# Optimization experiments

Measured on AMD Instinct MI355X. Metric: run time of the kernel, lower is better.

The kernel has to match this reference:

```python
import jax, jax.numpy as jnp
import numpy as np

N_ATOMS = 20000
N_CG = 1000
N_EDGES = 200000
FEAT = 128
N_RBF = 20
N_CONV = 3
CUTOFF = 5.0
EPS = 1e-15


def swish(x):
    return x * jax.nn.sigmoid(x)


def preprocess_r(r):
    # r: (n, 3) -> dist (n,), unit (n, 3)
    d = jnp.sqrt((r * r + EPS).sum(-1))
    return d, r / d[:, None]


def dist_embed(d, W, b):
    # PainnRadialBasis (learnable_k=False) + Dense + cosine envelope
    k = jnp.arange(1, N_RBF + 1, dtype=d.dtype)
    rbf = jnp.sin(k[None, :] * jnp.pi * d[:, None] / CUTOFF) / d[:, None]
    env = 0.5 * (jnp.cos(jnp.pi * d / CUTOFF) + 1.0) * (d < CUTOFF).astype(d.dtype)
    return (rbf @ W + b) * env[:, None]


def scatter_mean(x, idx, n):
    s = jax.ops.segment_sum(x, idx, num_segments=n)
    cnt = jax.ops.segment_sum(jnp.ones(idx.shape[0], x.dtype), idx, num_segments=n)
    cnt = jnp.maximum(cnt, 1.0)
    return s / cnt.reshape((n,) + (1,) * (x.ndim - 1))


def cg_encoder(z, xyz, cg_xyz, mapping, nbr_list, embed,
               msg_W1, msg_b1, msg_W2, msg_b2, msg_distW, msg_distb,
               upd_U, upd_V, upd_W1, upd_b1, upd_W2, upd_b2,
               cg_W1, cg_b1, cg_W2, cg_b2, cg_distW, cg_distb):
    s = embed[z]                                     # (N, F)
    v = jnp.zeros((s.shape[0], FEAT, 3), s.dtype)    # (N, F, 3)
    src, dst = nbr_list[:, 0], nbr_list[:, 1]
    r_ij = xyz[dst] - xyz[src]
    r_iI = xyz - cg_xyz[mapping]
    d_ij, u_ij = preprocess_r(r_ij)
    d_iI, u_iI = preprocess_r(r_iI)

    S_I = None
    V_I = None
    for i in range(N_CONV):
        # ---- MessageBlock ----
        phi = swish(s @ msg_W1[i] + msg_b1[i]) @ msg_W2[i] + msg_b2[i]          # (N, 3F)
        w_s = dist_embed(d_ij, msg_distW[i], msg_distb[i])                      # (E, 3F)
        inv = (phi[dst] * w_s).reshape(-1, 3, FEAT)                             # (E, 3, F)
        dv_ij = inv[:, 2, :, None] * u_ij[:, None, :] + inv[:, 0, :, None] * v[dst]
        s = s + jax.ops.segment_sum(inv[:, 1, :], src, num_segments=N_ATOMS)
        v = v + jax.ops.segment_sum(dv_ij, src, num_segments=N_ATOMS)
        # ---- UpdateBlock ----
        u_v = jnp.einsum('nfd,fg->ngd', v, upd_U[i])
        v_v = jnp.einsum('nfd,fg->ngd', v, upd_V[i])
        v_v_norm = jnp.sqrt((v_v * v_v + EPS).sum(-1))                          # (N, F)
        stack = swish(jnp.concatenate([s, v_v_norm], -1) @ upd_W1[i] + upd_b1[i]) @ upd_W2[i] + upd_b2[i]
        a_vv = stack[:, :FEAT, None]
        a_sv = stack[:, FEAT:2 * FEAT]
        a_ss = stack[:, 2 * FEAT:]
        v = v + u_v * a_vv
        s = s + (u_v * v_v).sum(-1) * a_sv + a_ss
        # ---- init CG features after first conv ----
        if i == 0:
            S_I = scatter_mean(s, mapping, N_CG)
            V_I = jnp.zeros((N_CG, FEAT, 3), s.dtype)
        # ---- ContractiveMessageBlock ----
        phi_cg = swish(s @ cg_W1[i] + cg_b1[i]) @ cg_W2[i] + cg_b2[i]           # (N, 3F)
        w_cg = dist_embed(d_iI, cg_distW[i], cg_distb[i])
        inv_cg = (phi_cg * w_cg).reshape(-1, 3, FEAT)
        dv_iI = inv_cg[:, 2, :, None] * u_iI[:, None, :] + inv_cg[:, 0, :, None] * v
        S_I = S_I + scatter_mean(inv_cg[:, 1, :], mapping, N_CG)
        V_I = V_I + scatter_mean(dv_iI, mapping, N_CG)
    return S_I


def setup_inputs() -> dict:
    key = jax.random.key(0)
    ks = jax.random.split(key, 20)
    p = lambda i, shape: jax.random.normal(ks[i], shape, jnp.float32) * 0.05
    return {
        'z': jax.random.randint(ks[0], (N_ATOMS,), 1, 100),
        'xyz': jax.random.normal(ks[1], (N_ATOMS, 3), jnp.float32),
        'cg_xyz': jax.random.normal(ks[2], (N_CG, 3), jnp.float32),
        'mapping': jax.random.randint(ks[3], (N_ATOMS,), 0, N_CG),
        'nbr_list': jax.random.randint(ks[4], (N_EDGES, 2), 0, N_ATOMS),
        'embed': p(5, (100, FEAT)).at[0].set(0.0),  # padding_idx=0
        'msg_W1': p(6, (N_CONV, FEAT, FEAT)), 'msg_b1': jnp.zeros((N_CONV, FEAT)),
        'msg_W2': p(7, (N_CONV, FEAT, 3 * FEAT)), 'msg_b2': jnp.zeros((N_CONV, 3 * FEAT)),
        'msg_distW': p(8, (N_CONV, N_RBF, 3 * FEAT)), 'msg_distb': jnp.zeros((N_CONV, 3 * FEAT)),
        'upd_U': p(9, (N_CONV, FEAT, FEAT)), 'upd_V': p(10, (N_CONV, FEAT, FEAT)),
        'upd_W1': p(11, (N_CONV, 2 * FEAT, FEAT)), 'upd_b1': jnp.zeros((N_CONV, FEAT)),
        'upd_W2': p(12, (N_CONV, FEAT, 3 * FEAT)), 'upd_b2': jnp.zeros((N_CONV, 3 * FEAT)),
        'cg_W1': p(13, (N_CONV, FEAT, FEAT)), 'cg_b1': jnp.zeros((N_CONV, FEAT)),
        'cg_W2': p(14, (N_CONV, FEAT, 3 * FEAT)), 'cg_b2': jnp.zeros((N_CONV, 3 * FEAT)),
        'cg_distW': p(15, (N_CONV, N_RBF, 3 * FEAT)), 'cg_distb': jnp.zeros((N_CONV, 3 * FEAT)),
    }


def reference(z, xyz, cg_xyz, mapping, nbr_list, embed,
              msg_W1, msg_b1, msg_W2, msg_b2, msg_distW, msg_distb,
              upd_U, upd_V, upd_W1, upd_b1, upd_W2, upd_b2,
              cg_W1, cg_b1, cg_W2, cg_b2, cg_distW, cg_distb):
    return cg_encoder(z, xyz, cg_xyz, mapping, nbr_list, embed,
                      msg_W1, msg_b1, msg_W2, msg_b2, msg_distW, msg_distb,
                      upd_U, upd_V, upd_W1, upd_b1, upd_W2, upd_b2,
                      cg_W1, cg_b1, cg_W2, cg_b2, cg_distW, cg_distb)
```

## Files before the change

kernel.cpp:

```cpp
#include <hip/hip_runtime.h>
#include <math.h>

#define N_ATOMS 20000
#define N_CG    1000
#define N_EDGES 200000
#define FEAT    128
#define NRBF    20
#define NCONV   3
#define CUTOFF  5.0f
#define PLANE   (N_ATOMS * FEAT)
#define PI_F    3.14159265358979323846f
#define LDH     130

#define PACK_PER_CONV 212992

typedef __attribute__((ext_vector_type(8))) short bf16x8;
typedef __attribute__((ext_vector_type(4))) float f32x4;

__device__ __forceinline__ void split2(float x, ushort& h, ushort& l)
{
    unsigned u  = __float_as_uint(x);
    unsigned hb = (u + 0x7FFFu + ((u >> 16) & 1u)) & 0xFFFF0000u;
    float    hf = __uint_as_float(hb);
    float    lf = x - hf;
    unsigned ul = __float_as_uint(lf);
    h = (ushort)(hb >> 16);
    l = (ushort)((ul + 0x7FFFu + ((ul >> 16) & 1u)) >> 16);
}

__device__ __forceinline__ void splitv8(const float* hv, bf16x8& ah, bf16x8& al)
{
#pragma unroll
    for (int j = 0; j < 8; ++j) {
        ushort h, l;
        split2(hv[j], h, l);
        ah[j] = (short)h; al[j] = (short)l;
    }
}

#define MFMA3(ACC, AH_, AL_, BH_, BL_)                                              \
    ACC = __builtin_amdgcn_mfma_f32_16x16x32_bf16(AH_, BH_, ACC, 0, 0, 0);          \
    ACC = __builtin_amdgcn_mfma_f32_16x16x32_bf16(AH_, BL_, ACC, 0, 0, 0);          \
    ACC = __builtin_amdgcn_mfma_f32_16x16x32_bf16(AL_, BH_, ACC, 0, 0, 0);

template<int K1, int N2>
__global__ __launch_bounds__(256)
void mlp_fused(const ushort* __restrict__ AH, const ushort* __restrict__ AL,
               const ushort* __restrict__ B1h, const ushort* __restrict__ B1l,
               const float* __restrict__ b1,
               const ushort* __restrict__ B2h, const ushort* __restrict__ B2l,
               const float* __restrict__ b2, int bcol0,
               float* __restrict__ C)
{
    __shared__ float Hs[32 * LDH];
    const int tid  = threadIdx.x;
    const int lane = tid & 63;
    const int w    = tid >> 6;
    const int wm   = w & 1, wn = w >> 1;
    const int m0   = blockIdx.x * 32;
    const int l15  = lane & 15;
    const int koff = (lane >> 4) * 8;
    const int rowb = wm * 16;
    const int q4   = (lane >> 4) * 4;

    f32x4 acc1[4];
#pragma unroll
    for (int j = 0; j < 4; ++j) acc1[j] = (f32x4){0.f, 0.f, 0.f, 0.f};
    for (int k0 = 0; k0 < K1; k0 += 32) {
        size_t aa = (size_t)(m0 + rowb + l15) * K1 + k0 + koff;
        bf16x8 ah = *reinterpret_cast<const bf16x8*>(AH + aa);
        bf16x8 al = *reinterpret_cast<const bf16x8*>(AL + aa);
#pragma unroll
        for (int nf = 0; nf < 4; ++nf) {
            size_t ba = (size_t)(wn * 64 + nf * 16 + l15) * K1 + k0 + koff;
            bf16x8 bh = *reinterpret_cast<const bf16x8*>(B1h + ba);
            bf16x8 bl = *reinterpret_cast<const bf16x8*>(B1l + ba);
            MFMA3(acc1[nf], ah, al, bh, bl);
        }
    }
#pragma unroll
    for (int nf = 0; nf < 4; ++nf) {
        int col = wn * 64 + nf * 16 + l15;
        float bv = b1[col];
#pragma unroll
        for (int r = 0; r < 4; ++r) {
            float x = acc1[nf][r] + bv;
            x = x / (1.f + __expf(-x));
            Hs[(rowb + q4 + r) * LDH + col] = x;
        }
    }
    __syncthreads();

    constexpr int NF2  = N2 / 32;
    constexpr int WCOL = N2 / 2;
    f32x4 acc2[NF2];
#pragma unroll
    for (int j = 0; j < NF2; ++j) acc2[j] = (f32x4){0.f, 0.f, 0.f, 0.f};
    for (int k0 = 0; k0 < 128; k0 += 32) {
        const float* hp = &Hs[(rowb + l15) * LDH + k0 + koff];
        float hv[8];
#pragma unroll
        for (int j = 0; j < 4; ++j) hv[j] = hp[j];
#pragma unroll
        for (int j = 0; j < 4; ++j) hv[4 + j] = hp[4 + j];
        bf16x8 ah, al;
        splitv8(hv, ah, al);
#pragma unroll
        for (int nf = 0; nf < NF2; ++nf) {
            size_t ba = (size_t)(wn * WCOL + nf * 16 + l15) * 128 + k0 + koff;
            bf16x8 bh = *reinterpret_cast<const bf16x8*>(B2h + ba);
            bf16x8 bl = *reinterpret_cast<const bf16x8*>(B2l + ba);
            MFMA3(acc2[nf], ah, al, bh, bl);
        }
    }
#pragma unroll
    for (int nf = 0; nf < NF2; ++nf) {
        int col = wn * WCOL + nf * 16 + l15;
        float bv = b2 ? b2[bcol0 + col] : 0.f;
#pragma unroll
        for (int r = 0; r < 4; ++r) {
            int row = m0 + rowb + q4 + r;
            C[(size_t)row * N2 + col] = acc2[nf][r] + bv;
        }
    }
}

__global__ __launch_bounds__(256)
void gemm_vnorm(const ushort* __restrict__ vHp, const ushort* __restrict__ vLp,
                const ushort* __restrict__ Bh, const ushort* __restrict__ Bl,
                float* __restrict__ vv,
                ushort* __restrict__ CcatH, ushort* __restrict__ CcatL)
{
    const int tid  = threadIdx.x;
    const int lane = tid & 63;
    const int w    = tid >> 6;
    const int wm   = w & 1, wn = w >> 1;
    const int m0   = blockIdx.x * 32;
    const int l15  = lane & 15;
    const int koff = (lane >> 4) * 8;
    const int rowb = wm * 16;
    const int q4   = (lane >> 4) * 4;

    f32x4 acc[3][4];
#pragma unroll
    for (int d = 0; d < 3; ++d)
#pragma unroll
        for (int j = 0; j < 4; ++j) acc[d][j] = (f32x4){0.f, 0.f, 0.f, 0.f};

    for (int k0 = 0; k0 < 128; k0 += 32) {
        bf16x8 ah[3], al[3];
#pragma unroll
        for (int d = 0; d < 3; ++d) {
            size_t aa = (size_t)d * PLANE + (size_t)(m0 + rowb + l15) * 128 + k0 + koff;
            ah[d] = *reinterpret_cast<const bf16x8*>(vHp + aa);
            al[d] = *reinterpret_cast<const bf16x8*>(vLp + aa);
        }
#pragma unroll
        for (int nf = 0; nf < 4; ++nf) {
            size_t ba = (size_t)(wn * 64 + nf * 16 + l15) * 128 + k0 + koff;
            bf16x8 bh = *reinterpret_cast<const bf16x8*>(Bh + ba);
            bf16x8 bl = *reinterpret_cast<const bf16x8*>(Bl + ba);
#pragma unroll
            for (int d = 0; d < 3; ++d) {
                MFMA3(acc[d][nf], ah[d], al[d], bh, bl);
            }
        }
    }
#pragma unroll
    for (int nf = 0; nf < 4; ++nf) {
        int col = wn * 64 + nf * 16 + l15;
#pragma unroll
        for (int r = 0; r < 4; ++r) {
            int row = m0 + rowb + q4 + r;
            int idx = row * FEAT + col;
            float x = acc[0][nf][r], y = acc[1][nf][r], z = acc[2][nf][r];
            vv[idx] = x; vv[PLANE + idx] = y; vv[2 * PLANE + idx] = z;
            float nrm = sqrtf(x * x + y * y + z * z + 3e-15f);
            ushort h, l;
            split2(nrm, h, l);
            CcatH[(size_t)row * 256 + 128 + col] = h;
            CcatL[(size_t)row * 256 + 128 + col] = l;
        }
    }
}

__global__ __launch_bounds__(256)
void gemm_u_update(const ushort* __restrict__ vHp, const ushort* __restrict__ vLp,
                   const ushort* __restrict__ Bh, const ushort* __restrict__ Bl,
                   const float* __restrict__ vv, const float* __restrict__ stack,
                   float* __restrict__ s, float* __restrict__ v,
                   ushort* __restrict__ sH, ushort* __restrict__ sL)
{
    const int tid  = threadIdx.x;
    const int lane = tid & 63;
    const int w    = tid >> 6;
    const int wm   = w & 1, wn = w >> 1;
    const int m0   = blockIdx.x * 32;
    const int l15  = lane & 15;
    const int koff = (lane >> 4) * 8;
    const int rowb = wm * 16;
    const int q4   = (lane >> 4) * 4;

    f32x4 acc[3][4];
#pragma unroll
    for (int d = 0; d < 3; ++d)
#pragma unroll
        for (int j = 0; j < 4; ++j) acc[d][j] = (f32x4){0.f, 0.f, 0.f, 0.f};

    for (int k0 = 0; k0 < 128; k0 += 32) {
        bf16x8 ah[3], al[3];
#pragma unroll
        for (int d = 0; d < 3; ++d) {
            size_t aa = (size_t)d * PLANE + (size_t)(m0 + rowb + l15) * 128 + k0 + koff;
            ah[d] = *reinterpret_cast<const bf16x8*>(vHp + aa);
            al[d] = *reinterpret_cast<const bf16x8*>(vLp + aa);
        }
#pragma unroll
        for (int nf = 0; nf < 4; ++nf) {
            size_t ba = (size_t)(wn * 64 + nf * 16 + l15) * 128 + k0 + koff;
            bf16x8 bh = *reinterpret_cast<const bf16x8*>(Bh + ba);
            bf16x8 bl = *reinterpret_cast<const bf16x8*>(Bl + ba);
#pragma unroll
            for (int d = 0; d < 3; ++d) {
                MFMA3(acc[d][nf], ah[d], al[d], bh, bl);
            }
        }
    }
    ushort* vHo = const_cast<ushort*>(vHp);
    ushort* vLo = const_cast<ushort*>(vLp);
#pragma unroll
    for (int nf = 0; nf < 4; ++nf) {
        int col = wn * 64 + nf * 16 + l15;
#pragma unroll
        for (int r = 0; r < 4; ++r) {
            int row = m0 + rowb + q4 + r;
            int idx = row * FEAT + col;
            const float* st = stack + (size_t)row * 384 + col;
            float avv = st[0], asv = st[128], ass = st[256];
            float u0 = acc[0][nf][r], u1 = acc[1][nf][r], u2 = acc[2][nf][r];
            float w0 = vv[idx], w1 = vv[PLANE + idx], w2 = vv[2 * PLANE + idx];
            float dot = u0 * w0 + u1 * w1 + u2 * w2;
            float n0 = v[idx]             + u0 * avv;
            float n1 = v[PLANE + idx]     + u1 * avv;
            float n2 = v[2 * PLANE + idx] + u2 * avv;
            v[idx] = n0; v[PLANE + idx] = n1; v[2 * PLANE + idx] = n2;
            ushort h, l;
            split2(n0, h, l); vHo[idx] = h;             vLo[idx] = l;
            split2(n1, h, l); vHo[PLANE + idx] = h;     vLo[PLANE + idx] = l;
            split2(n2, h, l); vHo[2 * PLANE + idx] = h; vLo[2 * PLANE + idx] = l;
            float ns = s[idx] + dot * asv + ass;
            s[idx] = ns;
            split2(ns, h, l); sH[idx] = h; sL[idx] = l;
        }
    }
}

__global__ void k_pack_all(const float* __restrict__ msg_W1, const float* __restrict__ msg_W2,
                           const float* __restrict__ upd_V,  const float* __restrict__ upd_W1,
                           const float* __restrict__ upd_W2, const float* __restrict__ upd_U,
                           const float* __restrict__ cg_W1,  const float* __restrict__ cg_W2,
                           ushort* __restrict__ Bh, ushort* __restrict__ Bl)
{
    const int wid = blockIdx.y, conv = blockIdx.z;
    const float* W; int K, N, ldw, col0; size_t off;
    switch (wid) {
        case 0: W = msg_W1 + (size_t)conv * 16384; K = 128; N = 128; ldw = 128; col0 = 0;   off = 0;      break;
        case 1: W = msg_W2 + (size_t)conv * 49152; K = 128; N = 384; ldw = 384; col0 = 0;   off = 16384;  break;
        case 2: W = upd_V  + (size_t)conv * 16384; K = 128; N = 128; ldw = 128; col0 = 0;   off = 65536;  break;
        case 3: W = upd_W1 + (size_t)conv * 32768; K = 256; N = 128; ldw = 128; col0 = 0;   off = 81920;  break;
        case 4: W = upd_W2 + (size_t)conv * 49152; K = 128; N = 384; ldw = 384; col0 = 0;   off = 114688; break;
        case 5: W = upd_U  + (size_t)conv * 16384; K = 128; N = 128; ldw = 128; col0 = 0;   off = 163840; break;
        case 6: W = cg_W1  + (size_t)conv * 16384; K = 128; N = 128; ldw = 128; col0 = 0;   off = 180224; break;
        default:W = cg_W2  + (size_t)conv * 49152; K = 128; N = 128; ldw = 384; col0 = 128; off = 196608; break;
    }
    off += (size_t)conv * PACK_PER_CONV;
    int idx = blockIdx.x * 256 + threadIdx.x;
    if (idx >= K * N) return;
    int k = idx & (K - 1);
    int n = idx >> ((K == 256) ? 8 : 7);
    ushort h, l;
    split2(W[(size_t)k * ldw + col0 + n], h, l);
    Bh[off + (size_t)n * K + k] = h;
    Bl[off + (size_t)n * K + k] = l;
}

__global__ void k_s_init(const int* __restrict__ z, const float* __restrict__ embed,
                         float* __restrict__ s, ushort* __restrict__ sH, ushort* __restrict__ sL)
{
    int idx = blockIdx.x * blockDim.x + threadIdx.x;
    if (idx >= PLANE) return;
    int n = idx >> 7, g = idx & 127;
    float e = embed[z[n] * FEAT + g];
    s[idx] = e;
    ushort h, l;
    split2(e, h, l);
    sH[idx] = h; sL[idx] = l;
}

__global__ void k_atom_geo(const int* __restrict__ mapping,
                           const float* __restrict__ xyz, const float* __restrict__ cg_xyz,
                           float* __restrict__ rbf_a, float* __restrict__ env_a,
                           float* __restrict__ cnt)
{
    int n = blockIdx.x * blockDim.x + threadIdx.x;
    if (n >= N_ATOMS) return;
    int m = mapping[n];
    float dx = xyz[n * 3 + 0] - cg_xyz[m * 3 + 0];
    float dy = xyz[n * 3 + 1] - cg_xyz[m * 3 + 1];
    float dz = xyz[n * 3 + 2] - cg_xyz[m * 3 + 2];
    float d = sqrtf(dx * dx + dy * dy + dz * dz + 3e-15f);
    float env = (d < CUTOFF) ? 0.5f * (cosf(PI_F * d / CUTOFF) + 1.f) : 0.f;
    env_a[n] = env;
    float s = env / d;
#pragma unroll
    for (int k = 0; k < NRBF; ++k)
        rbf_a[n * NRBF + k] = sinf((k + 1) * PI_F * d / CUTOFF) * s;
    atomicAdd(&cnt[m], 1.f);
}

__global__ void k_deg(const int* __restrict__ nbr, int* __restrict__ deg)
{
    int e = blockIdx.x * blockDim.x + threadIdx.x;
    if (e < N_EDGES) atomicAdd(&deg[nbr[2 * e]], 1);
}

__global__ __launch_bounds__(1024)
void k_scan(const int* __restrict__ deg, int* __restrict__ rowptr)
{
    __shared__ int sh[1024];
    const int chunk = (N_ATOMS + 1023) / 1024;
    int t = threadIdx.x;
    int base = t * chunk;
    int sum = 0;
    for (int i = 0; i < chunk; ++i) {
        int idx = base + i;
        if (idx < N_ATOMS) sum += deg[idx];
    }
    sh[t] = sum;
    __syncthreads();
    for (int off = 1; off < 1024; off <<= 1) {
        int val = (t >= off) ? sh[t - off] : 0;
        __syncthreads();
        sh[t] += val;
        __syncthreads();
    }
    int run = (t == 0) ? 0 : sh[t - 1];
    for (int i = 0; i < chunk; ++i) {
        int idx = base + i;
        if (idx < N_ATOMS) { rowptr[idx] = run; run += deg[idx]; }
    }
}

__global__ void k_fill(const int* __restrict__ nbr, const float* __restrict__ xyz,
                       const int* __restrict__ rowptr, int* __restrict__ cursor,
                       int* __restrict__ rec_dst, float4* __restrict__ rec_u4,
                       float* __restrict__ rec_rbf)
{
    int e = blockIdx.x * blockDim.x + threadIdx.x;
    if (e >= N_EDGES) return;
    int src = nbr[2 * e], dst = nbr[2 * e + 1];
    int pos = atomicAdd(&cursor[src], 1);
    int q = rowptr[src] + pos;
    float dx = xyz[dst * 3 + 0] - xyz[src * 3 + 0];
    float dy = xyz[dst * 3 + 1] - xyz[src * 3 + 1];
    float dz = xyz[dst * 3 + 2] - xyz[src * 3 + 2];
    float d = sqrtf(dx * dx + dy * dy + dz * dz + 3e-15f);
    float env = (d < CUTOFF) ? 0.5f * (cosf(PI_F * d / CUTOFF) + 1.f) : 0.f;
    rec_dst[q] = dst;
    rec_u4[q] = make_float4(dx / d, dy / d, dz / d, env);
    float sc = env / d;
#pragma unroll
    for (int k = 0; k < NRBF; ++k)
        rec_rbf[(size_t)q * NRBF + k] = sinf((k + 1) * PI_F * d / CUTOFF) * sc;
}

#define EDGE_BLOCKS 2500
__global__ __launch_bounds__(512, 2)
void k_edge_seg(const int* __restrict__ rowptr, const int* __restrict__ deg,
                const int* __restrict__ rec_dst, const float4* __restrict__ rec_u4,
                const float* __restrict__ rec_rbf,
                const float* __restrict__ phi,
                const float* __restrict__ v_in, float* __restrict__ v_out,
                float* __restrict__ s,
                ushort* __restrict__ vH, ushort* __restrict__ vL,
                ushort* __restrict__ CcatH, ushort* __restrict__ CcatL,
                const float* __restrict__ distW, const float* __restrict__ distb)
{
    const int tid    = threadIdx.x;
    const int slot   = tid >> 7;
    const int f      = tid & 127;
    const int slot_g = blockIdx.x * 4 + slot;
    const int nslots = EDGE_BLOCKS * 4;

    float wx[21], wy[21], wz[21];
#pragma unroll
    for (int k = 0; k < NRBF; ++k) {
        wx[k] = distW[k * 384 + f];
        wy[k] = distW[k * 384 + 128 + f];
        wz[k] = distW[k * 384 + 256 + f];
    }
    wx[20] = distb[f];
    wy[20] = distb[128 + f];
    wz[20] = distb[256 + f];
#pragma unroll
    for (int k = 0; k < 21; ++k) {
        asm volatile("" : "+v"(wx[k]), "+v"(wy[k]), "+v"(wz[k]));
    }

    for (int a = slot_g; a < N_ATOMS; a += nslots) {
        const int beg = rowptr[a];
        const int end = beg + deg[a];
        float s_acc = 0.f, vx = 0.f, vy = 0.f, vz = 0.f;

        for (int p = beg; p < end; p += 2) {
            const int  has2 = (p + 1 < end);
            const int  p1   = has2 ? p + 1 : p;
            const float m1  = has2 ? 1.f : 0.f;

            float4 u40 = rec_u4[p];
            float4 u41 = rec_u4[p1];
            int dst0 = rec_dst[p];
            int dst1 = rec_dst[p1];

            const float* ph0 = phi + (size_t)dst0 * 384 + f;
            const float* ph1 = phi + (size_t)dst1 * 384 + f;
            float p00 = ph0[0], p01 = ph0[128], p02 = ph0[256];
            float p10 = ph1[0], p11 = ph1[128], p12 = ph1[256];
            int di0 = dst0 * FEAT + f;
            int di1 = dst1 * FEAT + f;
            float v0x = v_in[di0], v0y = v_in[PLANE + di0], v0z = v_in[2 * PLANE + di0];
            float v1x = v_in[di1], v1y = v_in[PLANE + di1], v1z = v_in[2 * PLANE + di1];
            const float4* rb0 = reinterpret_cast<const float4*>(rec_rbf + (size_t)p  * NRBF);
            const float4* rb1 = reinterpret_cast<const float4*>(rec_rbf + (size_t)p1 * NRBF);
            float4 a0 = rb0[0], a1 = rb0[1], a2 = rb0[2], a3 = rb0[3], a4 = rb0[4];
            float4 b0 = rb1[0], b1 = rb1[1], b2 = rb1[2], b3 = rb1[3], b4 = rb1[4];

            const float rr0[21] = {a0.x, a0.y, a0.z, a0.w, a1.x, a1.y, a1.z, a1.w,
                                   a2.x, a2.y, a2.z, a2.w, a3.x, a3.y, a3.z, a3.w,
                                   a4.x, a4.y, a4.z, a4.w, u40.w};
            const float rr1[21] = {b0.x, b0.y, b0.z, b0.w, b1.x, b1.y, b1.z, b1.w,
                                   b2.x, b2.y, b2.z, b2.w, b3.x, b3.y, b3.z, b3.w,
                                   b4.x, b4.y, b4.z, b4.w, u41.w};
            float w00 = 0.f, w01 = 0.f, w02 = 0.f;
            float w10 = 0.f, w11 = 0.f, w12 = 0.f;
#pragma unroll
            for (int k = 0; k < 21; ++k) {
                w00 += rr0[k] * wx[k];
                w01 += rr0[k] * wy[k];
                w02 += rr0[k] * wz[k];
                w10 += rr1[k] * wx[k];
                w11 += rr1[k] * wy[k];
                w12 += rr1[k] * wz[k];
            }
            float i00 = p00 * w00, i01 = p01 * w01, i02 = p02 * w02;
            float i10 = (p10 * w10) * m1, i11 = (p11 * w11) * m1, i12 = (p12 * w12) * m1;
            vx += i02 * u40.x + i00 * v0x;
            vy += i02 * u40.y + i00 * v0y;
            vz += i02 * u40.z + i00 * v0z;
            s_acc += i01;
            vx += i12 * u41.x + i10 * v1x;
            vy += i12 * u41.y + i10 * v1y;
            vz += i12 * u41.z + i10 * v1z;
            s_acc += i11;
        }

        int si = a * FEAT + f;
        float ns = s[si] + s_acc;
        s[si] = ns;
        float nx = v_in[si]             + vx;
        float ny = v_in[PLANE + si]     + vy;
        float nz = v_in[2 * PLANE + si] + vz;
        v_out[si] = nx; v_out[PLANE + si] = ny; v_out[2 * PLANE + si] = nz;
        ushort h, l;
        split2(nx, h, l); vH[si] = h;             vL[si] = l;
        split2(ny, h, l); vH[PLANE + si] = h;     vL[PLANE + si] = l;
        split2(nz, h, l); vH[2 * PLANE + si] = h; vL[2 * PLANE + si] = l;
        split2(ns, h, l);
        CcatH[(size_t)a * 256 + f] = h;
        CcatL[(size_t)a * 256 + f] = l;
    }
}

__global__ __launch_bounds__(128)
void k_cg_msg(const int* __restrict__ mapping, const float* __restrict__ phi_mid,
              const float* __restrict__ rbf_a, const float* __restrict__ env_a,
              const float* __restrict__ distW, const float* __restrict__ distb,
              const float* __restrict__ s_add, float* __restrict__ S_acc)
{
    int n = blockIdx.x;
    float env = env_a[n];
    int f = threadIdx.x;
    if (env == 0.f && s_add == nullptr) return;
    float val = s_add ? s_add[n * FEAT + f] : 0.f;
    if (env != 0.f) {
        __shared__ float sh_rbf[NRBF];
        if (f < NRBF) sh_rbf[f] = rbf_a[n * NRBF + f];
        __syncthreads();
        float w1 = 0.f;
#pragma unroll
        for (int k = 0; k < NRBF; ++k)
            w1 += sh_rbf[k] * distW[k * 384 + 128 + f];
        w1 += distb[128 + f] * env;
        val += phi_mid[n * FEAT + f] * w1;
    }
    atomicAdd(&S_acc[mapping[n] * FEAT + f], val);
}

__global__ void k_finalize(const float* __restrict__ S_acc, const float* __restrict__ cnt,
                           float* __restrict__ out, int add)
{
    int idx = blockIdx.x * blockDim.x + threadIdx.x;
    if (idx >= N_CG * FEAT) return;
    float val = S_acc[idx] / fmaxf(cnt[idx >> 7], 1.f);
    if (add) out[idx] += val;
    else     out[idx] = val;
}

extern "C" void kernel_launch(void* const* d_in, const int* in_sizes, int n_in,
                              void* d_out, int out_size, void* d_ws, size_t ws_size,
                              hipStream_t stream)
{
    const int*   z        = (const int*)d_in[0];
    const float* xyz      = (const float*)d_in[1];
    const float* cg_xyz   = (const float*)d_in[2];
    const int*   mapping  = (const int*)d_in[3];
    const int*   nbr      = (const int*)d_in[4];
    const float* embed    = (const float*)d_in[5];
    const float* msg_W1   = (const float*)d_in[6];
    const float* msg_b1   = (const float*)d_in[7];
    const float* msg_W2   = (const float*)d_in[8];
    const float* msg_b2   = (const float*)d_in[9];
    const float* msg_dW   = (const float*)d_in[10];
    const float* msg_db   = (const float*)d_in[11];
    const float* upd_U    = (const float*)d_in[12];
    const float* upd_V    = (const float*)d_in[13];
    const float* upd_W1   = (const float*)d_in[14];
    const float* upd_b1   = (const float*)d_in[15];
    const float* upd_W2   = (const float*)d_in[16];
    const float* upd_b2   = (const float*)d_in[17];
    const float* cg_W1    = (const float*)d_in[18];
    const float* cg_b1    = (const float*)d_in[19];
    const float* cg_W2    = (const float*)d_in[20];
    const float* cg_b2    = (const float*)d_in[21];
    const float* cg_dW    = (const float*)d_in[22];
    const float* cg_db    = (const float*)d_in[23];
    float* out = (float*)d_out;

    float* ws = (float*)d_ws;
    size_t o = 0;
    float* s      = ws + o; o += PLANE;
    float* vA     = ws + o; o += 3 * PLANE;
    float* vB     = ws + o; o += 3 * PLANE;
    float* uv     = ws + o; o += PLANE;
    float* phi    = ws + o; o += (size_t)N_ATOMS * 384;
    float* Cpk    = ws + o; o += (size_t)N_ATOMS * 256;
    float* spk    = ws + o; o += PLANE;
    float* vpk    = ws + o; o += 3 * PLANE;
    float4* rec_u4 = (float4*)(ws + o); o += (size_t)N_EDGES * 4;
    float* rec_rbf = ws + o; o += (size_t)N_EDGES * NRBF;
    int*   rec_dst = (int*)(ws + o); o += N_EDGES;
    float* rbf_a  = ws + o; o += (size_t)N_ATOMS * NRBF;
    float* env_a  = ws + o; o += N_ATOMS;
    float* cnt    = ws + o; o += N_CG;
    float* S_acc  = ws + o; o += N_CG * FEAT;
    int*   deg    = (int*)(ws + o); o += N_ATOMS;
    int*   rowptr = (int*)(ws + o); o += N_ATOMS;
    int*   cursor = (int*)(ws + o); o += N_ATOMS;
    ushort* packH = (ushort*)(ws + o); o += (size_t)NCONV * PACK_PER_CONV / 2;
    ushort* packL = (ushort*)(ws + o); o += (size_t)NCONV * PACK_PER_CONV / 2;

    ushort* CcatH = (ushort*)Cpk; ushort* CcatL = CcatH + (size_t)N_ATOMS * 256;
    ushort* sH = (ushort*)spk;  ushort* sL = sH + PLANE;
    ushort* vH = (ushort*)vpk;  ushort* vL = vH + 3 * PLANE;

    hipMemsetAsync(vA, 0, sizeof(float) * 3 * PLANE, stream);
    hipMemsetAsync(cnt, 0, sizeof(float) * N_CG, stream);
    hipMemsetAsync(deg, 0, sizeof(int) * N_ATOMS, stream);
    hipMemsetAsync(cursor, 0, sizeof(int) * N_ATOMS, stream);
    k_pack_all<<<dim3(192, 8, 3), 256, 0, stream>>>(msg_W1, msg_W2, upd_V, upd_W1,
                                                    upd_W2, upd_U, cg_W1, cg_W2,
                                                    packH, packL);
    k_s_init<<<(PLANE + 255) / 256, 256, 0, stream>>>(z, embed, s, sH, sL);
    k_atom_geo<<<(N_ATOMS + 255) / 256, 256, 0, stream>>>(mapping, xyz, cg_xyz,
                                                          rbf_a, env_a, cnt);
    k_deg<<<(N_EDGES + 255) / 256, 256, 0, stream>>>(nbr, deg);
    k_scan<<<1, 1024, 0, stream>>>(deg, rowptr);
    k_fill<<<(N_EDGES + 255) / 256, 256, 0, stream>>>(nbr, xyz, rowptr, cursor,
                                                      rec_dst, rec_u4, rec_rbf);

    float* v_cur = vA;
    float* v_nxt = vB;

    for (int i = 0; i < NCONV; ++i) {
        const float* mb1 = msg_b1 + (size_t)i * FEAT;
        const float* mb2 = msg_b2 + (size_t)i * 384;
        const float* mdW = msg_dW + (size_t)i * NRBF * 384;
        const float* mdb = msg_db + (size_t)i * 384;
        const float* ub1 = upd_b1 + (size_t)i * FEAT;
        const float* ub2 = upd_b2 + (size_t)i * 384;
        const float* cb1 = cg_b1  + (size_t)i * FEAT;
        const float* cb2 = cg_b2  + (size_t)i * 384;
        const float* cdW = cg_dW  + (size_t)i * NRBF * 384;
        const float* cdb = cg_db  + (size_t)i * 384;
        const size_t pb  = (size_t)i * PACK_PER_CONV;

        mlp_fused<128, 384><<<625, 256, 0, stream>>>(
            sH, sL, packH + pb + 0, packL + pb + 0, mb1,
            packH + pb + 16384, packL + pb + 16384, mb2, 0, phi);
        k_edge_seg<<<EDGE_BLOCKS, 512, 0, stream>>>(rowptr, deg, rec_dst, rec_u4,
                                                    rec_rbf, phi, v_cur, v_nxt, s,
                                                    vH, vL, CcatH, CcatL, mdW, mdb);
        float* vv = v_cur;

        gemm_vnorm<<<625, 256, 0, stream>>>(vH, vL, packH + pb + 65536,
                                            packL + pb + 65536, vv, CcatH, CcatL);
        mlp_fused<256, 384><<<625, 256, 0, stream>>>(
            CcatH, CcatL, packH + pb + 81920, packL + pb + 81920, ub1,
            packH + pb + 114688, packL + pb + 114688, ub2, 0, phi);
        gemm_u_update<<<625, 256, 0, stream>>>(vH, vL, packH + pb + 163840,
                                               packL + pb + 163840, vv, phi,
                                               s, v_nxt, sH, sL);

        mlp_fused<128, 128><<<625, 256, 0, stream>>>(
            sH, sL, packH + pb + 180224, packL + pb + 180224, cb1,
            packH + pb + 196608, packL + pb + 196608, cb2, 128, uv);
        hipMemsetAsync(S_acc, 0, sizeof(float) * N_CG * FEAT, stream);
        k_cg_msg<<<N_ATOMS, 128, 0, stream>>>(mapping, uv, rbf_a, env_a, cdW, cdb,
                                              (i == 0) ? s : nullptr, S_acc);
        k_finalize<<<(N_CG * FEAT + 255) / 256, 256, 0, stream>>>(S_acc, cnt, out,
                                                                  i == 0 ? 0 : 1);

        float* tmp = v_nxt;
        v_nxt = v_cur;
        v_cur = tmp;
    }
}
```

Measured before the change: 1.363 ms.

## Fuse update block into one kernel and drop fp32 v buffers for bf16 split pairs

```diff
diff --git a/kernel.cpp b/kernel.cpp
--- a/kernel.cpp
+++ b/kernel.cpp
@@ -28,6 +28,12 @@
     l = (ushort)((ul + 0x7FFFu + ((ul >> 16) & 1u)) >> 16);
 }
 
+__device__ __forceinline__ float recon(const ushort* __restrict__ H,
+                                       const ushort* __restrict__ L, size_t i)
+{
+    return __uint_as_float((unsigned)H[i] << 16) + __uint_as_float((unsigned)L[i] << 16);
+}
+
 __device__ __forceinline__ void splitv8(const float* hv, bf16x8& ah, bf16x8& al)
 {
 #pragma unroll
@@ -126,11 +132,23 @@
 }
 
 __global__ __launch_bounds__(256)
-void gemm_vnorm(const ushort* __restrict__ vHp, const ushort* __restrict__ vLp,
-                const ushort* __restrict__ Bh, const ushort* __restrict__ Bl,
-                float* __restrict__ vv,
-                ushort* __restrict__ CcatH, ushort* __restrict__ CcatL)
-{
+void k_update_mega(const ushort* __restrict__ vHp, const ushort* __restrict__ vLp,
+                   const ushort* __restrict__ catH, const ushort* __restrict__ catL,
+                   const ushort* __restrict__ BVh, const ushort* __restrict__ BVl,
+                   const ushort* __restrict__ W1h, const ushort* __restrict__ W1l,
+                   const float*  __restrict__ b1,
+                   const ushort* __restrict__ W2h, const ushort* __restrict__ W2l,
+                   const float*  __restrict__ b2,
+                   const ushort* __restrict__ BUh, const ushort* __restrict__ BUl,
+                   float* __restrict__ s,
+                   ushort* __restrict__ sH, ushort* __restrict__ sL)
+{
+    __shared__ __align__(16) char smem[16640 + 49152];
+    float*  Hs  = (float*)smem;
+    float*  stk = (float*)(smem + 16640);
+    ushort* nH  = (ushort*)(smem + 16640);
+    ushort* nL  = (ushort*)(smem + 16640 + 8192);
+
     const int tid  = threadIdx.x;
     const int lane = tid & 63;
     const int w    = tid >> 6;
@@ -141,12 +159,14 @@
     const int rowb = wm * 16;
     const int q4   = (lane >> 4) * 4;
 
-    f32x4 acc[3][4];
+    f32x4 accV[3][4], accU[3][4];
 #pragma unroll
     for (int d = 0; d < 3; ++d)
 #pragma unroll
-        for (int j = 0; j < 4; ++j) acc[d][j] = (f32x4){0.f, 0.f, 0.f, 0.f};
-
+        for (int j = 0; j < 4; ++j) {
+            accV[d][j] = (f32x4){0.f, 0.f, 0.f, 0.f};
+            accU[d][j] = (f32x4){0.f, 0.f, 0.f, 0.f};
+        }
     for (int k0 = 0; k0 < 128; k0 += 32) {
         bf16x8 ah[3], al[3];
 #pragma unroll
@@ -158,11 +178,17 @@
 #pragma unroll
         for (int nf = 0; nf < 4; ++nf) {
             size_t ba = (size_t)(wn * 64 + nf * 16 + l15) * 128 + k0 + koff;
-            bf16x8 bh = *reinterpret_cast<const bf16x8*>(Bh + ba);
-            bf16x8 bl = *reinterpret_cast<const bf16x8*>(Bl + ba);
+            bf16x8 bvh = *reinterpret_cast<const bf16x8*>(BVh + ba);
+            bf16x8 bvl = *reinterpret_cast<const bf16x8*>(BVl + ba);
+            bf16x8 buh = *reinterpret_cast<const bf16x8*>(BUh + ba);
+            bf16x8 bul = *reinterpret_cast<const bf16x8*>(BUl + ba);
 #pragma unroll
             for (int d = 0; d < 3; ++d) {
-                MFMA3(acc[d][nf], ah[d], al[d], bh, bl);
+                MFMA3(accV[d][nf], ah[d], al[d], bvh, bvl);
+            }
+#pragma unroll
+            for (int d = 0; d < 3; ++d) {
+                MFMA3(accU[d][nf], ah[d], al[d], buh, bul);
             }
         }
     }
@@ -171,61 +197,81 @@
         int col = wn * 64 + nf * 16 + l15;
 #pragma unroll
         for (int r = 0; r < 4; ++r) {
-            int row = m0 + rowb + q4 + r;
-            int idx = row * FEAT + col;
-            float x = acc[0][nf][r], y = acc[1][nf][r], z = acc[2][nf][r];
-            vv[idx] = x; vv[PLANE + idx] = y; vv[2 * PLANE + idx] = z;
+            int lrow = rowb + q4 + r;
+            float x = accV[0][nf][r], y = accV[1][nf][r], z = accV[2][nf][r];
             float nrm = sqrtf(x * x + y * y + z * z + 3e-15f);
             ushort h, l;
             split2(nrm, h, l);
-            CcatH[(size_t)row * 256 + 128 + col] = h;
-            CcatL[(size_t)row * 256 + 128 + col] = l;
-        }
-    }
-}
-
-__global__ __launch_bounds__(256)
-void gemm_u_update(const ushort* __restrict__ vHp, const ushort* __restrict__ vLp,
-                   const ushort* __restrict__ Bh, const ushort* __restrict__ Bl,
-                   const float* __restrict__ vv, const float* __restrict__ stack,
-                   float* __restrict__ s, float* __restrict__ v,
-                   ushort* __restrict__ sH, ushort* __restrict__ sL)
-{
-    const int tid  = threadIdx.x;
-    const int lane = tid & 63;
-    const int w    = tid >> 6;
-    const int wm   = w & 1, wn = w >> 1;
-    const int m0   = blockIdx.x * 32;
-    const int l15  = lane & 15;
-    const int koff = (lane >> 4) * 8;
-    const int rowb = wm * 16;
-    const int q4   = (lane >> 4) * 4;
-
-    f32x4 acc[3][4];
-#pragma unroll
-    for (int d = 0; d < 3; ++d)
-#pragma unroll
-        for (int j = 0; j < 4; ++j) acc[d][j] = (f32x4){0.f, 0.f, 0.f, 0.f};
-
+            nH[lrow * 128 + col] = h;
+            nL[lrow * 128 + col] = l;
+        }
+    }
+    __syncthreads();
+
+    f32x4 acc1[4];
+#pragma unroll
+    for (int j = 0; j < 4; ++j) acc1[j] = (f32x4){0.f, 0.f, 0.f, 0.f};
+    for (int k0 = 0; k0 < 256; k0 += 32) {
+        bf16x8 ah, al;
+        if (k0 < 128) {
+            size_t aa = (size_t)(m0 + rowb + l15) * 128 + k0 + koff;
+            ah = *reinterpret_cast<const bf16x8*>(catH + aa);
+            al = *reinterpret_cast<const bf16x8*>(catL + aa);
+        } else {
+            int la = (rowb + l15) * 128 + (k0 - 128) + koff;
+            ah = *reinterpret_cast<const bf16x8*>(nH + la);
+            al = *reinterpret_cast<const bf16x8*>(nL + la);
+        }
+#pragma unroll
+        for (int nf = 0; nf < 4; ++nf) {
+            size_t ba = (size_t)(wn * 64 + nf * 16 + l15) * 256 + k0 + koff;
+            bf16x8 bh = *reinterpret_cast<const bf16x8*>(W1h + ba);
+            bf16x8 bl = *reinterpret_cast<const bf16x8*>(W1l + ba);
+            MFMA3(acc1[nf], ah, al, bh, bl);
+        }
+    }
+#pragma unroll
+    for (int nf = 0; nf < 4; ++nf) {
+        int col = wn * 64 + nf * 16 + l15;
+        float bv = b1[col];
+#pragma unroll
+        for (int r = 0; r < 4; ++r) {
+            float x = acc1[nf][r] + bv;
+            x = x / (1.f + __expf(-x));
+            Hs[(rowb + q4 + r) * LDH + col] = x;
+        }
+    }
+    __syncthreads();
+
+    f32x4 acc2[12];
+#pragma unroll
+    for (int j = 0; j < 12; ++j) acc2[j] = (f32x4){0.f, 0.f, 0.f, 0.f};
     for (int k0 = 0; k0 < 128; k0 += 32) {
-        bf16x8 ah[3], al[3];
-#pragma unroll
-        for (int d = 0; d < 3; ++d) {
-            size_t aa = (size_t)d * PLANE + (size_t)(m0 + rowb + l15) * 128 + k0 + koff;
-            ah[d] = *reinterpret_cast<const bf16x8*>(vHp + aa);
-            al[d] = *reinterpret_cast<const bf16x8*>(vLp + aa);
-        }
-#pragma unroll
-        for (int nf = 0; nf < 4; ++nf) {
-            size_t ba = (size_t)(wn * 64 + nf * 16 + l15) * 128 + k0 + koff;
-            bf16x8 bh = *reinterpret_cast<const bf16x8*>(Bh + ba);
-            bf16x8 bl = *reinterpret_cast<const bf16x8*>(Bl + ba);
-#pragma unroll
-            for (int d = 0; d < 3; ++d) {
-                MFMA3(acc[d][nf], ah[d], al[d], bh, bl);
-            }
-        }
-    }
+        const float* hp = &Hs[(rowb + l15) * LDH + k0 + koff];
+        float hv[8];
+#pragma unroll
+        for (int j = 0; j < 8; ++j) hv[j] = hp[j];
+        bf16x8 ah, al;
+        splitv8(hv, ah, al);
+#pragma unroll
+        for (int nf = 0; nf < 12; ++nf) {
+            size_t ba = (size_t)(wn * 192 + nf * 16 + l15) * 128 + k0 + koff;
+            bf16x8 bh = *reinterpret_cast<const bf16x8*>(W2h + ba);
+            bf16x8 bl = *reinterpret_cast<const bf16x8*>(W2l + ba);
+            MFMA3(acc2[nf], ah, al, bh, bl);
+        }
+    }
+#pragma unroll
+    for (int nf = 0; nf < 12; ++nf) {
+        int col = wn * 192 + nf * 16 + l15;
+        float bv = b2[col];
+#pragma unroll
+        for (int r = 0; r < 4; ++r) {
+            stk[(rowb + q4 + r) * 384 + col] = acc2[nf][r] + bv;
+        }
+    }
+    __syncthreads();
+
     ushort* vHo = const_cast<ushort*>(vHp);
     ushort* vLo = const_cast<ushort*>(vLp);
 #pragma unroll
@@ -233,17 +279,18 @@
         int col = wn * 64 + nf * 16 + l15;
 #pragma unroll
         for (int r = 0; r < 4; ++r) {
-            int row = m0 + rowb + q4 + r;
-            int idx = row * FEAT + col;
-            const float* st = stack + (size_t)row * 384 + col;
-            float avv = st[0], asv = st[128], ass = st[256];
-            float u0 = acc[0][nf][r], u1 = acc[1][nf][r], u2 = acc[2][nf][r];
-            float w0 = vv[idx], w1 = vv[PLANE + idx], w2 = vv[2 * PLANE + idx];
+            int lrow = rowb + q4 + r;
+            int row  = m0 + lrow;
+            int idx  = row * FEAT + col;
+            float avv = stk[lrow * 384 + col];
+            float asv = stk[lrow * 384 + 128 + col];
+            float ass = stk[lrow * 384 + 256 + col];
+            float u0 = accU[0][nf][r], u1 = accU[1][nf][r], u2 = accU[2][nf][r];
+            float w0 = accV[0][nf][r], w1 = accV[1][nf][r], w2 = accV[2][nf][r];
             float dot = u0 * w0 + u1 * w1 + u2 * w2;
-            float n0 = v[idx]             + u0 * avv;
-            float n1 = v[PLANE + idx]     + u1 * avv;
-            float n2 = v[2 * PLANE + idx] + u2 * avv;
-            v[idx] = n0; v[PLANE + idx] = n1; v[2 * PLANE + idx] = n2;
+            float n0 = recon(vHp, vLp, idx)                    + u0 * avv;
+            float n1 = recon(vHp, vLp, (size_t)PLANE + idx)    + u1 * avv;
+            float n2 = recon(vHp, vLp, (size_t)2 * PLANE + idx)+ u2 * avv;
             ushort h, l;
             split2(n0, h, l); vHo[idx] = h;             vLo[idx] = l;
             split2(n1, h, l); vHo[PLANE + idx] = h;     vLo[PLANE + idx] = l;
@@ -380,10 +427,10 @@
                 const int* __restrict__ rec_dst, const float4* __restrict__ rec_u4,
                 const float* __restrict__ rec_rbf,
                 const float* __restrict__ phi,
-                const float* __restrict__ v_in, float* __restrict__ v_out,
+                const ushort* __restrict__ vHi, const ushort* __restrict__ vLi,
+                ushort* __restrict__ vHo, ushort* __restrict__ vLo,
                 float* __restrict__ s,
-                ushort* __restrict__ vH, ushort* __restrict__ vL,
-                ushort* __restrict__ CcatH, ushort* __restrict__ CcatL,
+                ushort* __restrict__ catH, ushort* __restrict__ catL,
                 const float* __restrict__ distW, const float* __restrict__ distb)
 {
     const int tid    = threadIdx.x;
@@ -426,10 +473,14 @@
             const float* ph1 = phi + (size_t)dst1 * 384 + f;
             float p00 = ph0[0], p01 = ph0[128], p02 = ph0[256];
             float p10 = ph1[0], p11 = ph1[128], p12 = ph1[256];
-            int di0 = dst0 * FEAT + f;
-            int di1 = dst1 * FEAT + f;
-            float v0x = v_in[di0], v0y = v_in[PLANE + di0], v0z = v_in[2 * PLANE + di0];
-            float v1x = v_in[di1], v1y = v_in[PLANE + di1], v1z = v_in[2 * PLANE + di1];
+            size_t di0 = (size_t)dst0 * FEAT + f;
+            size_t di1 = (size_t)dst1 * FEAT + f;
+            float v0x = recon(vHi, vLi, di0);
+            float v0y = recon(vHi, vLi, PLANE + di0);
+            float v0z = recon(vHi, vLi, 2 * (size_t)PLANE + di0);
+            float v1x = recon(vHi, vLi, di1);
+            float v1y = recon(vHi, vLi, PLANE + di1);
+            float v1z = recon(vHi, vLi, 2 * (size_t)PLANE + di1);
             const float4* rb0 = reinterpret_cast<const float4*>(rec_rbf + (size_t)p  * NRBF);
             const float4* rb1 = reinterpret_cast<const float4*>(rec_rbf + (size_t)p1 * NRBF);
             float4 a0 = rb0[0], a1 = rb0[1], a2 = rb0[2], a3 = rb0[3], a4 = rb0[4];
@@ -464,20 +515,19 @@
             s_acc += i11;
         }
 
-        int si = a * FEAT + f;
+        size_t si = (size_t)a * FEAT + f;
         float ns = s[si] + s_acc;
         s[si] = ns;
-        float nx = v_in[si]             + vx;
-        float ny = v_in[PLANE + si]     + vy;
-        float nz = v_in[2 * PLANE + si] + vz;
-        v_out[si] = nx; v_out[PLANE + si] = ny; v_out[2 * PLANE + si] = nz;
+        float nx = recon(vHi, vLi, si)                    + vx;
+        float ny = recon(vHi, vLi, PLANE + si)            + vy;
+        float nz = recon(vHi, vLi, 2 * (size_t)PLANE + si)+ vz;
         ushort h, l;
-        split2(nx, h, l); vH[si] = h;             vL[si] = l;
-        split2(ny, h, l); vH[PLANE + si] = h;     vL[PLANE + si] = l;
-        split2(nz, h, l); vH[2 * PLANE + si] = h; vL[2 * PLANE + si] = l;
+        split2(nx, h, l); vHo[si] = h;             vLo[si] = l;
+        split2(ny, h, l); vHo[PLANE + si] = h;     vLo[PLANE + si] = l;
+        split2(nz, h, l); vHo[2 * PLANE + si] = h; vLo[2 * PLANE + si] = l;
         split2(ns, h, l);
-        CcatH[(size_t)a * 256 + f] = h;
-        CcatL[(size_t)a * 256 + f] = l;
+        catH[(size_t)a * 128 + f] = h;
+        catL[(size_t)a * 128 + f] = l;
     }
 }
 
@@ -549,13 +599,12 @@
     float* ws = (float*)d_ws;
     size_t o = 0;
     float* s      = ws + o; o += PLANE;
-    float* vA     = ws + o; o += 3 * PLANE;
-    float* vB     = ws + o; o += 3 * PLANE;
     float* uv     = ws + o; o += PLANE;
     float* phi    = ws + o; o += (size_t)N_ATOMS * 384;
-    float* Cpk    = ws + o; o += (size_t)N_ATOMS * 256;
+    float* catpk  = ws + o; o += PLANE;
     float* spk    = ws + o; o += PLANE;
-    float* vpk    = ws + o; o += 3 * PLANE;
+    float* vpkA   = ws + o; o += 3 * PLANE;
+    float* vpkB   = ws + o; o += 3 * PLANE;
     float4* rec_u4 = (float4*)(ws + o); o += (size_t)N_EDGES * 4;
     float* rec_rbf = ws + o; o += (size_t)N_EDGES * NRBF;
     int*   rec_dst = (int*)(ws + o); o += N_EDGES;
@@ -569,11 +618,12 @@
     ushort* packH = (ushort*)(ws + o); o += (size_t)NCONV * PACK_PER_CONV / 2;
     ushort* packL = (ushort*)(ws + o); o += (size_t)NCONV * PACK_PER_CONV / 2;
 
-    ushort* CcatH = (ushort*)Cpk; ushort* CcatL = CcatH + (size_t)N_ATOMS * 256;
+    ushort* catH = (ushort*)catpk; ushort* catL = catH + (size_t)N_ATOMS * 128;
     ushort* sH = (ushort*)spk;  ushort* sL = sH + PLANE;
-    ushort* vH = (ushort*)vpk;  ushort* vL = vH + 3 * PLANE;
-
-    hipMemsetAsync(vA, 0, sizeof(float) * 3 * PLANE, stream);
+    ushort* vHa = (ushort*)vpkA; ushort* vLa = vHa + 3 * (size_t)PLANE;
+    ushort* vHb = (ushort*)vpkB; ushort* vLb = vHb + 3 * (size_t)PLANE;
+
+    hipMemsetAsync(vpkA, 0, sizeof(float) * 3 * PLANE, stream);
     hipMemsetAsync(cnt, 0, sizeof(float) * N_CG, stream);
     hipMemsetAsync(deg, 0, sizeof(int) * N_ATOMS, stream);
     hipMemsetAsync(cursor, 0, sizeof(int) * N_ATOMS, stream);
@@ -588,8 +638,8 @@
     k_fill<<<(N_EDGES + 255) / 256, 256, 0, stream>>>(nbr, xyz, rowptr, cursor,
                                                       rec_dst, rec_u4, rec_rbf);
 
-    float* v_cur = vA;
-    float* v_nxt = vB;
+    ushort* vHc = vHa; ushort* vLc = vLa;
+    ushort* vHn = vHb; ushort* vLn = vLb;
 
     for (int i = 0; i < NCONV; ++i) {
         const float* mb1 = msg_b1 + (size_t)i * FEAT;
@@ -608,18 +658,19 @@
             sH, sL, packH + pb + 0, packL + pb + 0, mb1,
             packH + pb + 16384, packL + pb + 16384, mb2, 0, phi);
         k_edge_seg<<<EDGE_BLOCKS, 512, 0, stream>>>(rowptr, deg, rec_dst, rec_u4,
-                                                    rec_rbf, phi, v_cur, v_nxt, s,
-                                                    vH, vL, CcatH, CcatL, mdW, mdb);
-        float* vv = v_cur;
-
-        gemm_vnorm<<<625, 256, 0, stream>>>(vH, vL, packH + pb + 65536,
-                                            packL + pb + 65536, vv, CcatH, CcatL);
-        mlp_fused<256, 384><<<625, 256, 0, stream>>>(
-            CcatH, CcatL, packH + pb + 81920, packL + pb + 81920, ub1,
-            packH + pb + 114688, packL + pb + 114688, ub2, 0, phi);
-        gemm_u_update<<<625, 256, 0, stream>>>(vH, vL, packH + pb + 163840,
-                                               packL + pb + 163840, vv, phi,
-                                               s, v_nxt, sH, sL);
+                                                    rec_rbf, phi, vHc, vLc,
+                                                    vHn, vLn, s, catH, catL,
+                                                    mdW, mdb);
+
+        k_update_mega<<<625, 256, 0, stream>>>(
+            vHn, vLn, catH, catL,
+            packH + pb + 65536,  packL + pb + 65536,
+            packH + pb + 81920,  packL + pb + 81920,
+            ub1,
+            packH + pb + 114688, packL + pb + 114688,
+            ub2,
+            packH + pb + 163840, packL + pb + 163840,
+            s, sH, sL);
 
         mlp_fused<128, 128><<<625, 256, 0, stream>>>(
             sH, sL, packH + pb + 180224, packL + pb + 180224, cb1,
@@ -630,8 +681,8 @@
         k_finalize<<<(N_CG * FEAT + 255) / 256, 256, 0, stream>>>(S_acc, cnt, out,
                                                                   i == 0 ? 0 : 1);
 
-        float* tmp = v_nxt;
-        v_nxt = v_cur;
-        v_cur = tmp;
-    }
-}
+        ushort* th = vHn; ushort* tl = vLn;
+        vHn = vHc; vLn = vLc;
+        vHc = th;  vLc = tl;
+    }
+}
```

Measured after the change: 1.487 ms. 9.1% more time.
